# Optimization experiments

Hardware: AMD Instinct MI355X
Metric: run time of the kernel (lower is better)

The kernel has to match this reference:

```python
import jax, jax.numpy as jnp
import numpy as np

EMB = 512
HEADS = 8
B, T = 4, 1024


def setup_inputs() -> dict:
    key = jax.random.key(0)
    k1, k2, k3, k4, k5 = jax.random.split(key, 5)
    scale = 1.0 / np.sqrt(EMB)
    x = jax.random.normal(k1, (B, T, EMB), dtype=jnp.float32)
    # Linear(emb, emb*heads, bias=False) weights, stored as [in, out] for x @ W
    Wk = jax.random.normal(k2, (EMB, EMB * HEADS), dtype=jnp.float32) * scale
    Wq = jax.random.normal(k3, (EMB, EMB * HEADS), dtype=jnp.float32) * scale
    Wv = jax.random.normal(k4, (EMB, EMB * HEADS), dtype=jnp.float32) * scale
    Wu = jax.random.normal(k5, (EMB * HEADS, EMB), dtype=jnp.float32) * (1.0 / np.sqrt(EMB * HEADS))
    return {"x": x, "Wk": Wk, "Wq": Wq, "Wv": Wv, "Wu": Wu}


def reference(x, Wk, Wq, Wv, Wu):
    b, t, k = x.shape
    h = HEADS
    # projections -> [b, h, t, k]
    keys = (x @ Wk).reshape(b, t, h, k).transpose(0, 2, 1, 3)
    queries = (x @ Wq).reshape(b, t, h, k).transpose(0, 2, 1, 3)
    values = (x @ Wv).reshape(b, t, h, k).transpose(0, 2, 1, 3)
    # NOTE: original computes bmm(keys, queries^T): dot[i,j] = key_i . query_j
    dot = jnp.einsum('bhik,bhjk->bhij', keys, queries)  # [b,h,t,t]
    # mask_fn: only upper-triangle (offset=1) entries that are EXACTLY zero get -inf
    triu = jnp.triu(jnp.ones((t, t), dtype=bool), k=1)
    final_mask = triu & (dot == 0)
    dot = jnp.where(final_mask, -jnp.inf, dot)
    attn = jax.nn.softmax(dot, axis=-1)
    out = jnp.einsum('bhij,bhjk->bhik', attn, values)  # [b,h,t,k]
    out = out.transpose(0, 2, 1, 3).reshape(b, t, h * k)
    return out @ Wu
```

## Files before the change

kernel.cpp:

```cpp
#include <hip/hip_runtime.h>
#include <stdint.h>

typedef _Float16 f16x8 __attribute__((ext_vector_type(8)));
typedef float f32x4 __attribute__((ext_vector_type(4)));

__device__ __forceinline__ unsigned short f2h(float f) {
  _Float16 h = (_Float16)f;
  return __builtin_bit_cast(unsigned short, h);
}

#if __has_builtin(__builtin_amdgcn_global_load_lds)
#define HAVE_GLL 1
__device__ __forceinline__ void gload_lds16(const void* g, void* l) {
  auto gp = reinterpret_cast<const __attribute__((address_space(1))) void*>(
      reinterpret_cast<uintptr_t>(g));
  auto lp = reinterpret_cast<__attribute__((address_space(3))) void*>(
      reinterpret_cast<uintptr_t>(l));
  __builtin_amdgcn_global_load_lds(gp, lp, 16, 0, 0);
}
#else
#define HAVE_GLL 0
#endif

__device__ __forceinline__ void transpose_core(const float* in, unsigned short* out,
                                               int R, int C, int c0, int r0) {
  __shared__ float t[32][33];
  int tx = threadIdx.x & 31, ty = threadIdx.x >> 5;
#pragma unroll
  for (int i = 0; i < 32; i += 8)
    t[ty + i][tx] = in[(long)(r0 + ty + i) * C + (c0 + tx)];
  __syncthreads();
#pragma unroll
  for (int i = 0; i < 32; i += 8)
    out[(long)(c0 + ty + i) * R + (r0 + tx)] = f2h(t[tx][ty + i]);
}

__global__ __launch_bounds__(256) void k_setup(
    const float* __restrict__ x, const float* __restrict__ Wq, const float* __restrict__ Wk,
    const float* __restrict__ Wv, const float* __restrict__ Wu,
    unsigned short* __restrict__ Xh, unsigned short* __restrict__ Wqf,
    unsigned short* __restrict__ Wkf, unsigned short* __restrict__ Wvh,
    unsigned short* __restrict__ Wut) {
  int z = blockIdx.z;
  if (z == 2) {
    transpose_core(Wu, Wut, 4096, 512, blockIdx.y * 32, blockIdx.x * 32);
  } else {
    const float* in = (z == 0) ? Wq : (z == 1) ? Wk : (z == 3) ? x : Wv;
    unsigned short* o = (z == 0) ? Wqf : (z == 1) ? Wkf : (z == 3) ? Xh : Wvh;
    int i = (blockIdx.y * 128 + blockIdx.x) * 256 + threadIdx.x;
    float4 v = reinterpret_cast<const float4*>(in)[i];
    ushort4 u;
    u.x = f2h(v.x); u.y = f2h(v.y); u.z = f2h(v.z); u.w = f2h(v.w);
    reinterpret_cast<ushort4*>(o)[i] = u;
  }
}

template <int OUT, int BVU>
__device__ __forceinline__ void gemm_core(unsigned short* __restrict__ As,
                                          unsigned short* __restrict__ Bs,
                                          const unsigned short* __restrict__ A,
                                          const unsigned short* __restrict__ B,
                                          void* __restrict__ Cv, int K, int lda, int ldb,
                                          int ldc, long coff, int m0, int n0, int kbase) {
  int tid = threadIdx.x;
  int wid = tid >> 6, lane = tid & 63;
  int wm = (wid >> 1) * 64, wn = (wid & 1) * 64;
  int rq = lane >> 4, rl = lane & 15;

  f32x4 acc[4][4];
#pragma unroll
  for (int i = 0; i < 4; ++i)
#pragma unroll
    for (int j = 0; j < 4; ++j) acc[i][j] = (f32x4){0.f, 0.f, 0.f, 0.f};

#if HAVE_GLL
  int cg = (lane & 7) ^ ((lane >> 3) & 7);
  int rl8 = lane >> 3;
#endif

  for (int k0 = 0; k0 < K; k0 += 64) {
    long bko;
    if (BVU) {
      int kk = kbase + k0;
      bko = (long)(kk >> 10) * 2097152 + (kk & 1023);
    } else {
      bko = k0;
    }
    __syncthreads();
#if HAVE_GLL
#pragma unroll
    for (int t = 0; t < 4; ++t) {
      int r = wid * 32 + t * 8;
      gload_lds16(&A[(long)(m0 + r + rl8) * lda + k0 + cg * 8], &As[r * 64]);
      gload_lds16(&B[(long)(n0 + r + rl8) * ldb + bko + cg * 8], &Bs[r * 64]);
    }
#else
#pragma unroll
    for (int it = 0; it < 4; ++it) {
      int idx = tid + it * 256;
      int r = idx >> 3, c = idx & 7;
      int cs = c ^ (r & 7);
      *reinterpret_cast<uint4*>(&As[r * 64 + cs * 8]) =
          *reinterpret_cast<const uint4*>(&A[(long)(m0 + r) * lda + k0 + c * 8]);
      *reinterpret_cast<uint4*>(&Bs[r * 64 + cs * 8]) =
          *reinterpret_cast<const uint4*>(&B[(long)(n0 + r) * ldb + bko + c * 8]);
    }
#endif
    __syncthreads();
#pragma unroll
    for (int ks = 0; ks < 2; ++ks) {
      f16x8 af[4], bfr[4];
      int kc = ks * 4 + rq;
#pragma unroll
      for (int i = 0; i < 4; ++i) {
        int ra = wm + i * 16 + rl;
        af[i] = *reinterpret_cast<const f16x8*>(&As[ra * 64 + ((kc ^ (ra & 7)) << 3)]);
        int rb = wn + i * 16 + rl;
        bfr[i] = *reinterpret_cast<const f16x8*>(&Bs[rb * 64 + ((kc ^ (rb & 7)) << 3)]);
      }
#pragma unroll
      for (int i = 0; i < 4; ++i)
#pragma unroll
        for (int j = 0; j < 4; ++j)
          acc[i][j] = __builtin_amdgcn_mfma_f32_16x16x32_f16(af[i], bfr[j], acc[i][j], 0, 0, 0);
    }
  }

#pragma unroll
  for (int i = 0; i < 4; ++i)
#pragma unroll
    for (int j = 0; j < 4; ++j)
#pragma unroll
      for (int r = 0; r < 4; ++r) {
        int row = m0 + wm + i * 16 + rq * 4 + r;
        int col = n0 + wn + j * 16 + rl;
        float v = acc[i][j][r];
        if (OUT == 1)
          reinterpret_cast<unsigned short*>(Cv)[coff + (long)row * ldc + col] = f2h(v);
        else
          reinterpret_cast<float*>(Cv)[coff + (long)row * ldc + col] = v;
      }
}

#define DECL_LDS \
  __shared__ unsigned short As[128 * 64]; \
  __shared__ unsigned short Bs[128 * 64];

__global__ __launch_bounds__(256, 2) void k_gemm_w(
    const unsigned short* __restrict__ Wqf, const unsigned short* __restrict__ Wkf,
    const unsigned short* __restrict__ Wut, const unsigned short* __restrict__ Wvh,
    unsigned short* __restrict__ Gt, unsigned short* __restrict__ Wvut) {
  DECL_LDS
  int c = blockIdx.x, w = blockIdx.y;
  const unsigned short *A, *B;
  unsigned short* C;
  int t;
  if (w < 16) { A = Wqf + c * 512; B = Wkf + c * 512; C = Gt + (long)c * 262144; t = w; }
  else        { A = Wut + c * 512; B = Wvh + c * 512; C = Wvut + (long)c * 262144; t = w - 16; }
  gemm_core<1, 0>(As, Bs, A, B, C, 512, 4096, 4096, 512, 0, (t >> 2) * 128, (t & 3) * 128, 0);
}

__global__ __launch_bounds__(256, 2) void k_gemm_tv(
    const unsigned short* __restrict__ X, const unsigned short* __restrict__ Gt,
    const unsigned short* __restrict__ Wvut, unsigned short* __restrict__ T,
    unsigned short* __restrict__ VUt) {
  DECL_LDS
  int c = blockIdx.x, w = blockIdx.y;
  const unsigned short *A, *B;
  unsigned short* C;
  long coff;
  int m0, n0;
  if (w < 128) {
    A = X; B = Gt + (long)c * 262144; C = T;
    coff = (long)c * 512; m0 = (w >> 2) * 128; n0 = (w & 3) * 128;
  } else {
    int wp = w - 128;
    A = Wvut; B = X; C = VUt;
    coff = 0; m0 = (4 * c + (wp & 3)) * 128; n0 = (wp >> 2) * 128;
  }
  gemm_core<1, 0>(As, Bs, A, B, C, 512, 512, 512, 4096, coff, m0, n0, 0);
}

__global__ __launch_bounds__(256, 2) void k_gemm_s(
    const unsigned short* __restrict__ X, const unsigned short* __restrict__ T,
    unsigned short* __restrict__ Pb) {
  DECL_LDS
  int c = blockIdx.x, w = blockIdx.y;
  int z = c + 8 * (w >> 6), t = w & 63;
  int b = z >> 3, h = z & 7;
  gemm_core<1, 0>(As, Bs, T + (long)b * 4194304 + h * 512, X + (long)b * 524288, Pb,
                  512, 4096, 512, 8192, (long)b * 8388608 + h * 1024,
                  (t >> 3) * 128, (t & 7) * 128, 0);
}

__global__ __launch_bounds__(256, 2) void k_gemm_out(
    const unsigned short* __restrict__ Pb, const unsigned short* __restrict__ VUt,
    float* __restrict__ Opart) {
  DECL_LDS
  int c = blockIdx.x, w = blockIdx.y;
  int g = c + 8 * (w >> 4);
  int r = w & 15;
  int b = g >> 3, kc = (g >> 1) & 3, ih = g & 1;
  int y = ih * 4 + (r >> 2);
  int x = r & 3;
  gemm_core<0, 1>(As, Bs, Pb + (long)b * 8388608 + kc * 2048, VUt + (long)b * 1024,
                  Opart, 2048, 8192, 4096, 512,
                  (long)kc * 2097152 + (long)b * 524288, y * 128, x * 128, kc * 2048);
}

__global__ __launch_bounds__(256) void k_reduce(const float* __restrict__ Opart,
                                                float* __restrict__ out) {
  int i = blockIdx.x * 256 + threadIdx.x;
  float4 a = reinterpret_cast<const float4*>(Opart)[i];
  float4 b = reinterpret_cast<const float4*>(Opart + 2097152)[i];
  float4 c = reinterpret_cast<const float4*>(Opart + 4194304)[i];
  float4 d = reinterpret_cast<const float4*>(Opart + 6291456)[i];
  float4 o;
  o.x = (a.x + b.x) + (c.x + d.x);
  o.y = (a.y + b.y) + (c.y + d.y);
  o.z = (a.z + b.z) + (c.z + d.z);
  o.w = (a.w + b.w) + (c.w + d.w);
  reinterpret_cast<float4*>(out)[i] = o;
}

__global__ __launch_bounds__(256) void k_softmax_x(unsigned short* __restrict__ S) {
  int g = blockIdx.y * 4 + (threadIdx.x >> 6);
  int b = g >> 10, i = g & 1023;
  long base = (long)b * 8388608 + (long)i * 8192 + (long)blockIdx.x * 1024;
  int lane = threadIdx.x & 63;
  f16x8* p = reinterpret_cast<f16x8*>(S + base);
  f16x8 a = p[lane * 2], bb = p[lane * 2 + 1];
  float v[16];
#pragma unroll
  for (int q = 0; q < 8; ++q) { v[q] = (float)a[q]; v[8 + q] = (float)bb[q]; }
  float m = v[0];
#pragma unroll
  for (int q = 1; q < 16; ++q) m = fmaxf(m, v[q]);
#pragma unroll
  for (int o = 32; o; o >>= 1) m = fmaxf(m, __shfl_xor(m, o));
  float s = 0.f;
#pragma unroll
  for (int q = 0; q < 16; ++q) { v[q] = __expf(v[q] - m); s += v[q]; }
#pragma unroll
  for (int o = 32; o; o >>= 1) s += __shfl_xor(s, o);
  float inv = 1.0f / s;
  f16x8 oa, ob;
#pragma unroll
  for (int q = 0; q < 8; ++q) {
    oa[q] = (_Float16)(v[q] * inv);
    ob[q] = (_Float16)(v[8 + q] * inv);
  }
  p[lane * 2] = oa;
  p[lane * 2 + 1] = ob;
}

__global__ void k_sentinel(float* out, float v) { out[0] = v; }

extern "C" void kernel_launch(void* const* d_in, const int* in_sizes, int n_in,
                              void* d_out, int out_size, void* d_ws, size_t ws_size,
                              hipStream_t stream) {
  const float* x  = (const float*)d_in[0];
  const float* Wk = (const float*)d_in[1];
  const float* Wq = (const float*)d_in[2];
  const float* Wv = (const float*)d_in[3];
  const float* Wu = (const float*)d_in[4];
  float* out = (float*)d_out;

  const long SZ_X = 4096L * 512;
  const long SZ_W = 512L * 4096;
  const size_t NEED = 188743680;

  if (ws_size < NEED) {
    hipMemsetAsync(d_out, 0, (size_t)out_size * 4, stream);
    k_sentinel<<<1, 1, 0, stream>>>(out, (float)ws_size);
    return;
  }

  char* p = (char*)d_ws;
  unsigned short* Xbf  = (unsigned short*)p; p += SZ_X * 2;
  unsigned short* Wqf  = (unsigned short*)p; p += SZ_W * 2;
  unsigned short* Wkf  = (unsigned short*)p; p += SZ_W * 2;
  unsigned short* Wut  = (unsigned short*)p; p += SZ_W * 2;
  unsigned short* Wvut = (unsigned short*)p; p += SZ_W * 2;
  unsigned short* Gt   = (unsigned short*)p; p += 8L * 512 * 512 * 2;
  unsigned short* T    = (unsigned short*)p; p += 4096L * 4096 * 2;
  unsigned short* Pb   = (unsigned short*)p; p += 4096L * 8192 * 2;
  unsigned short* VUt  = (unsigned short*)p;
  unsigned short* Wvh  = VUt;
  float* Opart = (float*)T;

  k_setup<<<dim3(128, 16, 5), 256, 0, stream>>>(x, Wq, Wk, Wv, Wu, Xbf, Wqf, Wkf, Wvh, Wut);

  k_gemm_w<<<dim3(8, 32), 256, 0, stream>>>(Wqf, Wkf, Wut, Wvh, Gt, Wvut);

  k_gemm_tv<<<dim3(8, 256), 256, 0, stream>>>(Xbf, Gt, Wvut, T, VUt);

  k_gemm_s<<<dim3(8, 256), 256, 0, stream>>>(Xbf, T, Pb);

  k_softmax_x<<<dim3(8, 1024), 256, 0, stream>>>(Pb);

  k_gemm_out<<<dim3(8, 64), 256, 0, stream>>>(Pb, VUt, Opart);

  k_reduce<<<2048, 256, 0, stream>>>(Opart, out);
}
```

Measured before the change: 252.3 us.

## Fuse fp32-to-fp16 weight conversion into the weight GEMM kernel

Result: faster. 234.9 us (-6.9%).

```diff
diff --git a/kernel.cpp b/kernel.cpp
--- a/kernel.cpp
+++ b/kernel.cpp
@@ -21,39 +21,6 @@
 #else
 #define HAVE_GLL 0
 #endif
-
-__device__ __forceinline__ void transpose_core(const float* in, unsigned short* out,
-                                               int R, int C, int c0, int r0) {
-  __shared__ float t[32][33];
-  int tx = threadIdx.x & 31, ty = threadIdx.x >> 5;
-#pragma unroll
-  for (int i = 0; i < 32; i += 8)
-    t[ty + i][tx] = in[(long)(r0 + ty + i) * C + (c0 + tx)];
-  __syncthreads();
-#pragma unroll
-  for (int i = 0; i < 32; i += 8)
-    out[(long)(c0 + ty + i) * R + (r0 + tx)] = f2h(t[tx][ty + i]);
-}
-
-__global__ __launch_bounds__(256) void k_setup(
-    const float* __restrict__ x, const float* __restrict__ Wq, const float* __restrict__ Wk,
-    const float* __restrict__ Wv, const float* __restrict__ Wu,
-    unsigned short* __restrict__ Xh, unsigned short* __restrict__ Wqf,
-    unsigned short* __restrict__ Wkf, unsigned short* __restrict__ Wvh,
-    unsigned short* __restrict__ Wut) {
-  int z = blockIdx.z;
-  if (z == 2) {
-    transpose_core(Wu, Wut, 4096, 512, blockIdx.y * 32, blockIdx.x * 32);
-  } else {
-    const float* in = (z == 0) ? Wq : (z == 1) ? Wk : (z == 3) ? x : Wv;
-    unsigned short* o = (z == 0) ? Wqf : (z == 1) ? Wkf : (z == 3) ? Xh : Wvh;
-    int i = (blockIdx.y * 128 + blockIdx.x) * 256 + threadIdx.x;
-    float4 v = reinterpret_cast<const float4*>(in)[i];
-    ushort4 u;
-    u.x = f2h(v.x); u.y = f2h(v.y); u.z = f2h(v.z); u.w = f2h(v.w);
-    reinterpret_cast<ushort4*>(o)[i] = u;
-  }
-}
 
 template <int OUT, int BVU>
 __device__ __forceinline__ void gemm_core(unsigned short* __restrict__ As,
@@ -142,22 +109,120 @@
       }
 }
 
+__device__ __forceinline__ void w_core(unsigned short* __restrict__ As,
+                                       unsigned short* __restrict__ Bs,
+                                       const float* __restrict__ A32,
+                                       const float* __restrict__ B32,
+                                       unsigned short* __restrict__ C,
+                                       int lda, int ldb, bool atrans, int m0, int n0) {
+  int tid = threadIdx.x;
+  int wid = tid >> 6, lane = tid & 63;
+  int wm = (wid >> 1) * 64, wn = (wid & 1) * 64;
+  int rq = lane >> 4, rl = lane & 15;
+
+  f32x4 acc[4][4];
+#pragma unroll
+  for (int i = 0; i < 4; ++i)
+#pragma unroll
+    for (int j = 0; j < 4; ++j) acc[i][j] = (f32x4){0.f, 0.f, 0.f, 0.f};
+
+  for (int k0 = 0; k0 < 512; k0 += 64) {
+    __syncthreads();
+    if (!atrans) {
+#pragma unroll
+      for (int it = 0; it < 8; ++it) {
+        int idx = it * 256 + tid;
+        int r = idx >> 4, kq = idx & 15;
+        float4 v = *reinterpret_cast<const float4*>(&A32[(long)(m0 + r) * lda + k0 + kq * 4]);
+        ushort4 u;
+        u.x = f2h(v.x); u.y = f2h(v.y); u.z = f2h(v.z); u.w = f2h(v.w);
+        int cs = (kq >> 1) ^ (r & 7);
+        *reinterpret_cast<ushort4*>(&As[r * 64 + cs * 8 + (kq & 1) * 4]) = u;
+      }
+    } else {
+#pragma unroll
+      for (int it = 0; it < 32; ++it) {
+        int idx = it * 256 + tid;
+        int m = idx & 127, d = idx >> 7;
+        float v = A32[(long)(k0 + d) * 512 + m0 + m];
+        int cs = (d >> 3) ^ (m & 7);
+        As[m * 64 + cs * 8 + (d & 7)] = f2h(v);
+      }
+    }
+#pragma unroll
+    for (int it = 0; it < 8; ++it) {
+      int idx = it * 256 + tid;
+      int r = idx >> 4, kq = idx & 15;
+      float4 v = *reinterpret_cast<const float4*>(&B32[(long)(n0 + r) * ldb + k0 + kq * 4]);
+      ushort4 u;
+      u.x = f2h(v.x); u.y = f2h(v.y); u.z = f2h(v.z); u.w = f2h(v.w);
+      int cs = (kq >> 1) ^ (r & 7);
+      *reinterpret_cast<ushort4*>(&Bs[r * 64 + cs * 8 + (kq & 1) * 4]) = u;
+    }
+    __syncthreads();
+#pragma unroll
+    for (int ks = 0; ks < 2; ++ks) {
+      f16x8 af[4], bfr[4];
+      int kc = ks * 4 + rq;
+#pragma unroll
+      for (int i = 0; i < 4; ++i) {
+        int ra = wm + i * 16 + rl;
+        af[i] = *reinterpret_cast<const f16x8*>(&As[ra * 64 + ((kc ^ (ra & 7)) << 3)]);
+        int rb = wn + i * 16 + rl;
+        bfr[i] = *reinterpret_cast<const f16x8*>(&Bs[rb * 64 + ((kc ^ (rb & 7)) << 3)]);
+      }
+#pragma unroll
+      for (int i = 0; i < 4; ++i)
+#pragma unroll
+        for (int j = 0; j < 4; ++j)
+          acc[i][j] = __builtin_amdgcn_mfma_f32_16x16x32_f16(af[i], bfr[j], acc[i][j], 0, 0, 0);
+    }
+  }
+
+#pragma unroll
+  for (int i = 0; i < 4; ++i)
+#pragma unroll
+    for (int j = 0; j < 4; ++j)
+#pragma unroll
+      for (int r = 0; r < 4; ++r) {
+        int row = m0 + wm + i * 16 + rq * 4 + r;
+        int col = n0 + wn + j * 16 + rl;
+        C[(long)row * 512 + col] = f2h(acc[i][j][r]);
+      }
+}
+
 #define DECL_LDS \
   __shared__ unsigned short As[128 * 64]; \
   __shared__ unsigned short Bs[128 * 64];
 
-__global__ __launch_bounds__(256, 2) void k_gemm_w(
-    const unsigned short* __restrict__ Wqf, const unsigned short* __restrict__ Wkf,
-    const unsigned short* __restrict__ Wut, const unsigned short* __restrict__ Wvh,
-    unsigned short* __restrict__ Gt, unsigned short* __restrict__ Wvut) {
+__global__ __launch_bounds__(256, 2) void k_wsetup(
+    const float* __restrict__ x, const float* __restrict__ Wq, const float* __restrict__ Wk,
+    const float* __restrict__ Wv, const float* __restrict__ Wu,
+    unsigned short* __restrict__ Xh, unsigned short* __restrict__ Gt,
+    unsigned short* __restrict__ Wvut) {
   DECL_LDS
   int c = blockIdx.x, w = blockIdx.y;
-  const unsigned short *A, *B;
+  if (w >= 32) {
+    int i = ((w - 32) * 8 + c) * 256 + threadIdx.x;
+    float4 v = reinterpret_cast<const float4*>(x)[i];
+    ushort4 u;
+    u.x = f2h(v.x); u.y = f2h(v.y); u.z = f2h(v.z); u.w = f2h(v.w);
+    reinterpret_cast<ushort4*>(Xh)[i] = u;
+    return;
+  }
+  const float *A32, *B32;
   unsigned short* C;
+  int lda;
+  bool atrans;
   int t;
-  if (w < 16) { A = Wqf + c * 512; B = Wkf + c * 512; C = Gt + (long)c * 262144; t = w; }
-  else        { A = Wut + c * 512; B = Wvh + c * 512; C = Wvut + (long)c * 262144; t = w - 16; }
-  gemm_core<1, 0>(As, Bs, A, B, C, 512, 4096, 4096, 512, 0, (t >> 2) * 128, (t & 3) * 128, 0);
+  if (w < 16) {
+    A32 = Wq + c * 512; B32 = Wk + c * 512; C = Gt + (long)c * 262144;
+    lda = 4096; atrans = false; t = w;
+  } else {
+    A32 = Wu + (long)c * 262144; B32 = Wv + c * 512; C = Wvut + (long)c * 262144;
+    lda = 512; atrans = true; t = w - 16;
+  }
+  w_core(As, Bs, A32, B32, C, lda, 4096, atrans, (t >> 2) * 128, (t & 3) * 128);
 }
 
 __global__ __launch_bounds__(256, 2) void k_gemm_tv(
@@ -267,8 +332,7 @@
   float* out = (float*)d_out;
 
   const long SZ_X = 4096L * 512;
-  const long SZ_W = 512L * 4096;
-  const size_t NEED = 188743680;
+  const size_t NEED = 150994944;
 
   if (ws_size < NEED) {
     hipMemsetAsync(d_out, 0, (size_t)out_size * 4, stream);
@@ -278,20 +342,14 @@
 
   char* p = (char*)d_ws;
   unsigned short* Xbf  = (unsigned short*)p; p += SZ_X * 2;
-  unsigned short* Wqf  = (unsigned short*)p; p += SZ_W * 2;
-  unsigned short* Wkf  = (unsigned short*)p; p += SZ_W * 2;
-  unsigned short* Wut  = (unsigned short*)p; p += SZ_W * 2;
-  unsigned short* Wvut = (unsigned short*)p; p += SZ_W * 2;
+  unsigned short* Wvut = (unsigned short*)p; p += 8L * 512 * 512 * 2;
   unsigned short* Gt   = (unsigned short*)p; p += 8L * 512 * 512 * 2;
   unsigned short* T    = (unsigned short*)p; p += 4096L * 4096 * 2;
   unsigned short* Pb   = (unsigned short*)p; p += 4096L * 8192 * 2;
   unsigned short* VUt  = (unsigned short*)p;
-  unsigned short* Wvh  = VUt;
   float* Opart = (float*)T;
 
-  k_setup<<<dim3(128, 16, 5), 256, 0, stream>>>(x, Wq, Wk, Wv, Wu, Xbf, Wqf, Wkf, Wvh, Wut);
-
-  k_gemm_w<<<dim3(8, 32), 256, 0, stream>>>(Wqf, Wkf, Wut, Wvh, Gt, Wvut);
+  k_wsetup<<<dim3(8, 288), 256, 0, stream>>>(x, Wq, Wk, Wv, Wu, Xbf, Gt, Wvut);
 
   k_gemm_tv<<<dim3(8, 256), 256, 0, stream>>>(Xbf, Gt, Wvut, T, VUt);
 
```
